# Kernel tuning notes

Hardware: AMD Instinct MI355X
Metric: run time of the kernel (lower is better)

Reference implementation:

```python
import jax, jax.numpy as jnp
import numpy as np

N = 100000
E_RAND = 400000
IN_FEATS = 512
HID = 64
HEADS = 8
NUM_CLASSES = 40
SLOPE = 0.2  # DGL GATConv leaky_relu negative_slope


def setup_inputs() -> dict:
    key = jax.random.key(0)
    ks = jax.random.split(key, 12)
    features = jax.random.normal(ks[0], (N, IN_FEATS), dtype=jnp.float32)
    src_r = jax.random.randint(ks[1], (E_RAND,), 0, N)
    dst_r = jax.random.randint(ks[2], (E_RAND,), 0, N)
    loop = jnp.arange(N)
    src = jnp.concatenate([src_r, loop]).astype(jnp.int64)
    dst = jnp.concatenate([dst_r, loop]).astype(jnp.int64)
    def glorot(k, shape, fan_in):
        return jax.random.normal(k, shape, dtype=jnp.float32) * (1.0 / np.sqrt(fan_in))
    W1 = glorot(ks[3], (IN_FEATS, HEADS * HID), IN_FEATS)
    al1 = glorot(ks[4], (HEADS, HID), HID)
    ar1 = glorot(ks[5], (HEADS, HID), HID)
    b1 = jnp.zeros((HEADS * HID,), dtype=jnp.float32)
    W2 = glorot(ks[6], (HEADS * HID, HEADS * NUM_CLASSES), HEADS * HID)
    al2 = glorot(ks[7], (HEADS, NUM_CLASSES), NUM_CLASSES)
    ar2 = glorot(ks[8], (HEADS, NUM_CLASSES), NUM_CLASSES)
    b2 = jnp.zeros((HEADS * NUM_CLASSES,), dtype=jnp.float32)
    return {"features": features, "W1": W1, "al1": al1, "ar1": ar1, "b1": b1,
            "W2": W2, "al2": al2, "ar2": ar2, "b2": b2, "src": src, "dst": dst}


def gat_conv(x, W, al, ar, b, src, dst, heads, d_out):
    # x: [N, F_in] -> feat: [N, H, D]
    n = x.shape[0]
    feat = (x @ W).reshape(n, heads, d_out)
    el = jnp.sum(feat * al, axis=-1)  # [N, H]
    er = jnp.sum(feat * ar, axis=-1)  # [N, H]
    e = jax.nn.leaky_relu(el[src] + er[dst], SLOPE)  # [E, H]
    # segment softmax over incoming edges of each destination node
    emax = jax.ops.segment_max(e, dst, num_segments=n)
    a = jnp.exp(e - emax[dst])
    asum = jax.ops.segment_sum(a, dst, num_segments=n)
    alpha = a / asum[dst]  # [E, H]
    # weighted scatter-sum of source features
    out = jax.ops.segment_sum(feat[src] * alpha[:, :, None], dst, num_segments=n)
    return out + b.reshape(1, heads, d_out)  # [N, H, D]


def reference(features, W1, al1, ar1, b1, W2, al2, ar2, b2, src, dst):
    h = gat_conv(features, W1, al1, ar1, b1, src, dst, HEADS, HID)
    h = jax.nn.relu(h.reshape(N, HEADS * HID))  # flatten(1) + relu; dropout is eval-mode identity
    out = gat_conv(h, W2, al2, ar2, b2, src, dst, HEADS, NUM_CLASSES)
    return out.mean(axis=1)  # [N, num_classes]
```

## Files before the change

kernel.cpp:

```cpp
#include <hip/hip_runtime.h>
#include <cstdint>
#include <cstddef>

#define SLOPE 0.2f
#define HEADS 8

typedef __bf16 bf16_t;
typedef __bf16 bf16x8 __attribute__((ext_vector_type(8)));
typedef float f32x4 __attribute__((ext_vector_type(4)));

__global__ void cvt_w_t(const float* __restrict__ W, bf16_t* __restrict__ Bt, int K, int N) {
  int gid = blockIdx.x * blockDim.x + threadIdx.x;
  if (gid >= K * N) return;
  int nn = gid / K, kk = gid % K;
  Bt[gid] = (bf16_t)W[(size_t)kk * N + nn];
}

__global__ void cvt_wel2(const float* __restrict__ W2, const float* __restrict__ al2,
                         const float* __restrict__ ar2, bf16_t* __restrict__ W2t) {
  int gid = blockIdx.x * blockDim.x + threadIdx.x;
  if (gid >= 8 * 512) return;
  int h = gid >> 9, k = gid & 511;
  float a = 0.f, b = 0.f;
  for (int d = 0; d < 40; ++d) {
    float w = W2[(size_t)k * 320 + h * 40 + d];
    a = fmaf(w, al2[h * 40 + d], a);
    b = fmaf(w, ar2[h * 40 + d], b);
  }
  W2t[(size_t)(320 + h) * 512 + k] = (bf16_t)a;
  W2t[(size_t)(328 + h) * 512 + k] = (bf16_t)b;
}

__global__ __launch_bounds__(256) void gemm_af32(
    const float* __restrict__ A,
    const bf16_t* __restrict__ Bt,
    bf16_t* __restrict__ Cb,
    int M, int Nc, int K) {
  __shared__ __align__(16) unsigned char lds[49152];
  const int tid = threadIdx.x;
  const int wid = tid >> 6, lane = tid & 63;
  const int wm = wid >> 1, wn = wid & 1;
  const int bm = blockIdx.y * 128, bn = blockIdx.x * 128;
  const int quad = lane >> 4, lrow = lane & 15;

  f32x4 acc[4][4] = {};

  const int arow_in = 4 * wid + (lane >> 4);
  const int acol_src = ((lane & 15) * 4) ^ (((lane >> 4) + 4 * (wid & 1)) << 3);
  const int st_sub = wid * 8 + (lane >> 3);
  const int st_k = 8 * ((lane & 7) ^ (lane >> 3));
  const bf16_t* bSrc = Bt + (size_t)(bn + st_sub) * K + st_k;

  const int xorv = (lrow & 7) << 4;
  const int aRdRow = (wm * 64 + lrow) * 256;
  const int bRdBase = (wn * 64 + lrow) * 128 + 32768;

  for (int k0 = 0; k0 < K; k0 += 64) {
    if (k0) __syncthreads();
#pragma unroll
    for (int i = 0; i < 8; ++i) {
      int rg = bm + 16 * i + arow_in;
      rg = rg < M ? rg : M - 1;
      __builtin_amdgcn_global_load_lds(
          (const __attribute__((address_space(1))) void*)(A + (size_t)rg * K + k0 + acol_src),
          (__attribute__((address_space(3))) void*)(lds + (i * 4 + wid) * 1024), 16, 0, 0);
    }
#pragma unroll
    for (int i = 0; i < 4; ++i) {
      __builtin_amdgcn_global_load_lds(
          (const __attribute__((address_space(1))) void*)(bSrc + (size_t)i * 32 * K + k0),
          (__attribute__((address_space(3))) void*)(lds + 32768 + (i * 4 + wid) * 1024), 16, 0, 0);
    }
    __syncthreads();
#pragma unroll
    for (int kk = 0; kk < 2; ++kk) {
      bf16x8 af[4], bfr[4];
      const int kbA = (kk * 128 + quad * 32) ^ ((lrow & 7) << 5);
      const int kb = (kk * 64 + quad * 16) ^ xorv;
#pragma unroll
      for (int mf = 0; mf < 4; ++mf) {
        f32x4 lo = *(const f32x4*)(lds + aRdRow + mf * 4096 + kbA);
        f32x4 hi = *(const f32x4*)(lds + aRdRow + mf * 4096 + kbA + 16);
        bf16x8 t;
        t[0] = (bf16_t)lo[0]; t[1] = (bf16_t)lo[1]; t[2] = (bf16_t)lo[2]; t[3] = (bf16_t)lo[3];
        t[4] = (bf16_t)hi[0]; t[5] = (bf16_t)hi[1]; t[6] = (bf16_t)hi[2]; t[7] = (bf16_t)hi[3];
        af[mf] = t;
      }
#pragma unroll
      for (int nf = 0; nf < 4; ++nf)
        bfr[nf] = *(const bf16x8*)(lds + bRdBase + nf * 2048 + kb);
#pragma unroll
      for (int mf = 0; mf < 4; ++mf)
#pragma unroll
        for (int nf = 0; nf < 4; ++nf)
          acc[mf][nf] =
              __builtin_amdgcn_mfma_f32_16x16x32_bf16(af[mf], bfr[nf], acc[mf][nf], 0, 0, 0);
    }
  }

  const int crow0 = bm + wm * 64 + quad * 4;
  const int ccol0 = bn + wn * 64 + lrow;
#pragma unroll
  for (int mf = 0; mf < 4; ++mf) {
#pragma unroll
    for (int r2 = 0; r2 < 4; ++r2) {
      int row = crow0 + mf * 16 + r2;
      if (row < M) {
#pragma unroll
        for (int nf = 0; nf < 4; ++nf) {
          int col = ccol0 + nf * 16;
          if (col < Nc) Cb[(size_t)row * Nc + col] = (bf16_t)acc[mf][nf][r2];
        }
      }
    }
  }
}

template <bool HASEL>
__global__ __launch_bounds__(256) void gemm_bf16(
    const bf16_t* __restrict__ A,
    const bf16_t* __restrict__ Bt,
    bf16_t* __restrict__ Cb,
    float* __restrict__ elp, float* __restrict__ erp,
    int M, int NcFeat, int K) {
  __shared__ __align__(16) unsigned char lds[32768];
  const int tid = threadIdx.x;
  const int wid = tid >> 6, lane = tid & 63;
  const int wm = wid >> 1, wn = wid & 1;
  const int bm = blockIdx.y * 128, bn = blockIdx.x * 128;
  const int quad = lane >> 4, lrow = lane & 15;

  f32x4 acc[4][4] = {};

  const int st_sub = wid * 8 + (lane >> 3);
  const int st_k = 8 * ((lane & 7) ^ (lane >> 3));
  const bf16_t* aSrc = A + (size_t)(bm + st_sub) * K + st_k;
  const bf16_t* bSrc = Bt + (size_t)(bn + st_sub) * K + st_k;

  const int xorv = (lrow & 7) << 4;
  const int aRdBase = (wm * 64 + lrow) * 128;
  const int bRdBase = (wn * 64 + lrow) * 128 + 16384;

  for (int k0 = 0; k0 < K; k0 += 64) {
    if (k0) __syncthreads();
#pragma unroll
    for (int i = 0; i < 4; ++i) {
      __builtin_amdgcn_global_load_lds(
          (const __attribute__((address_space(1))) void*)(aSrc + (size_t)i * 32 * K + k0),
          (__attribute__((address_space(3))) void*)(lds + (i * 4 + wid) * 1024), 16, 0, 0);
    }
#pragma unroll
    for (int i = 0; i < 4; ++i) {
      __builtin_amdgcn_global_load_lds(
          (const __attribute__((address_space(1))) void*)(bSrc + (size_t)i * 32 * K + k0),
          (__attribute__((address_space(3))) void*)(lds + 16384 + (i * 4 + wid) * 1024), 16, 0, 0);
    }
    __syncthreads();
#pragma unroll
    for (int kk = 0; kk < 2; ++kk) {
      bf16x8 af[4], bfr[4];
      const int kb = (kk * 64 + quad * 16) ^ xorv;
#pragma unroll
      for (int mf = 0; mf < 4; ++mf)
        af[mf] = *(const bf16x8*)(lds + aRdBase + mf * 2048 + kb);
#pragma unroll
      for (int nf = 0; nf < 4; ++nf)
        bfr[nf] = *(const bf16x8*)(lds + bRdBase + nf * 2048 + kb);
#pragma unroll
      for (int mf = 0; mf < 4; ++mf)
#pragma unroll
        for (int nf = 0; nf < 4; ++nf)
          acc[mf][nf] =
              __builtin_amdgcn_mfma_f32_16x16x32_bf16(af[mf], bfr[nf], acc[mf][nf], 0, 0, 0);
    }
  }

  const int crow0 = bm + wm * 64 + quad * 4;
  const int ccol0 = bn + wn * 64 + lrow;
#pragma unroll
  for (int mf = 0; mf < 4; ++mf) {
#pragma unroll
    for (int r2 = 0; r2 < 4; ++r2) {
      int row = crow0 + mf * 16 + r2;
      if (row < M) {
#pragma unroll
        for (int nf = 0; nf < 4; ++nf) {
          int col = ccol0 + nf * 16;
          float v = acc[mf][nf][r2];
          if (col < NcFeat) {
            Cb[(size_t)row * NcFeat + col] = (bf16_t)v;
          } else if (HASEL) {
            if (col < NcFeat + 8) elp[(size_t)row * 8 + (col - NcFeat)] = v;
            else if (col < NcFeat + 16) erp[(size_t)row * 8 + (col - NcFeat - 8)] = v;
          }
        }
      }
    }
  }
}

__global__ void el_er_b(const bf16_t* __restrict__ featb, const float* __restrict__ al,
                        const float* __restrict__ ar, float* __restrict__ el,
                        float* __restrict__ er, int n, int D) {
  int gid = blockIdx.x * blockDim.x + threadIdx.x;
  if (gid >= n * HEADS) return;
  int node = gid >> 3, h = gid & 7;
  const bf16_t* f = featb + (size_t)node * HEADS * D + h * D;
  const float* alp = al + h * D;
  const float* arp = ar + h * D;
  float a = 0.f, b = 0.f;
  for (int d = 0; d < D; d += 8) {
    bf16x8 v = *(const bf16x8*)(f + d);
#pragma unroll
    for (int i = 0; i < 8; ++i) {
      float x = (float)v[i];
      a = fmaf(x, alp[d + i], a);
      b = fmaf(x, arp[d + i], b);
    }
  }
  el[gid] = a;
  er[gid] = b;
}

__global__ void count_deg(const int* __restrict__ dst, int* __restrict__ deg, int e) {
  int gid = blockIdx.x * blockDim.x + threadIdx.x;
  if (gid < e) atomicAdd(&deg[dst[gid]], 1);
}

__global__ void scan_block(const int* __restrict__ deg, int* __restrict__ incl,
                           int* __restrict__ bsum, int n) {
  __shared__ int tmp[256];
  int t = threadIdx.x;
  int gid = blockIdx.x * 256 + t;
  int v = (gid < n) ? deg[gid] : 0;
  tmp[t] = v;
  __syncthreads();
  for (int off = 1; off < 256; off <<= 1) {
    int x = (t >= off) ? tmp[t - off] : 0;
    __syncthreads();
    tmp[t] += x;
    __syncthreads();
  }
  if (gid < n) incl[gid] = tmp[t];
  if (t == 255) bsum[blockIdx.x] = tmp[255];
}

__global__ void scan_small(const int* __restrict__ bsum, int* __restrict__ bbase, int nb) {
  __shared__ int tmp[512];
  int t = threadIdx.x;
  int v = (t < nb) ? bsum[t] : 0;
  tmp[t] = v;
  __syncthreads();
  for (int off = 1; off < 512; off <<= 1) {
    int x = (t >= off) ? tmp[t - off] : 0;
    __syncthreads();
    tmp[t] += x;
    __syncthreads();
  }
  if (t < nb) bbase[t] = tmp[t] - v;
}

__global__ void finalize_offsets(const int* __restrict__ incl, const int* __restrict__ deg,
                                 const int* __restrict__ bbase, int* __restrict__ offsets,
                                 int n) {
  int gid = blockIdx.x * blockDim.x + threadIdx.x;
  if (gid >= n) return;
  int base = bbase[gid >> 8];
  offsets[gid] = incl[gid] - deg[gid] + base;
  if (gid == n - 1) offsets[n] = incl[gid] + base;
}

__global__ void scatter_edges(const int* __restrict__ src, const int* __restrict__ dst,
                              const int* __restrict__ offsets, int* __restrict__ cursor,
                              int* __restrict__ ssrc, int e) {
  int gid = blockIdx.x * blockDim.x + threadIdx.x;
  if (gid < e) {
    int d = dst[gid];
    int p = offsets[d] + atomicAdd(&cursor[d], 1);
    ssrc[p] = src[gid];
  }
}

__device__ inline void wave_softmax_stats(const float* __restrict__ el, float er_h, int h,
                                          int strip, const int* __restrict__ ssrc, int s0,
                                          int s1, float& m, float& ss) {
  m = -INFINITY;
  ss = 0.f;
  for (int j = s0 + strip; j < s1; j += 8) {
    int s = ssrc[j];
    float x = el[s * HEADS + h] + er_h;
    x = x > 0.f ? x : SLOPE * x;
    if (x > m) {
      ss = ss * __expf(m - x) + 1.f;
      m = x;
    } else {
      ss += __expf(x - m);
    }
  }
#pragma unroll
  for (int mask = 1; mask < 8; mask <<= 1) {
    float mo = __shfl_xor(m, mask, 64);
    float so = __shfl_xor(ss, mask, 64);
    float mn = fmaxf(m, mo);
    float e1 = (m == -INFINITY) ? 0.f : __expf(m - mn);
    float e2 = (mo == -INFINITY) ? 0.f : __expf(mo - mn);
    ss = ss * e1 + so * e2;
    m = mn;
  }
}

__global__ __launch_bounds__(256) void aggregate1(
    const bf16_t* __restrict__ featb, const float* __restrict__ el,
    const float* __restrict__ er, const int* __restrict__ offsets,
    const int* __restrict__ ssrc, const float* __restrict__ bias,
    bf16_t* __restrict__ outb, int n) {
  int wid = threadIdx.x >> 6, lane = threadIdx.x & 63;
  int node = blockIdx.x * 4 + wid;
  if (node >= n) return;
  int s0 = offsets[node], s1 = offsets[node + 1];
  int h = lane >> 3, strip = lane & 7;
  float er_h = er[node * HEADS + h];
  float m, ss;
  wave_softmax_stats(el, er_h, h, strip, ssrc, s0, s1, m, ss);
  float inv_ss = 1.f / ss;

  float acc[8] = {};
  for (int j = s0; j < s1; ++j) {
    int s = ssrc[j];
    float x = el[s * HEADS + h] + er_h;
    x = x > 0.f ? x : SLOPE * x;
    float alpha = __expf(x - m) * inv_ss;
    bf16x8 fv = *(const bf16x8*)(featb + (size_t)s * 512 + lane * 8);
#pragma unroll
    for (int i = 0; i < 8; ++i) acc[i] += alpha * (float)fv[i];
  }
  bf16x8 o;
#pragma unroll
  for (int i = 0; i < 8; ++i) {
    float v = acc[i] + bias[lane * 8 + i];
    o[i] = (bf16_t)fmaxf(v, 0.f);
  }
  *(bf16x8*)(outb + (size_t)node * 512 + lane * 8) = o;
}

__global__ __launch_bounds__(256) void aggregate2(
    const bf16_t* __restrict__ featb, const float* __restrict__ el,
    const float* __restrict__ er, const int* __restrict__ offsets,
    const int* __restrict__ ssrc, const float* __restrict__ bias,
    float* __restrict__ out, int n) {
  __shared__ float red[4][320];
  int wid = threadIdx.x >> 6, lane = threadIdx.x & 63;
  int node = blockIdx.x * 4 + wid;
  if (node >= n) return;
  int s0 = offsets[node], s1 = offsets[node + 1];
  int h = lane >> 3, strip = lane & 7;
  float er_h = er[node * HEADS + h];
  float m, ss;
  wave_softmax_stats(el, er_h, h, strip, ssrc, s0, s1, m, ss);
  float inv_ss = 1.f / ss;

  int alane0 = ((lane + 0 * 64) / 40) * 8;
  int alane1 = ((lane + 1 * 64) / 40) * 8;
  int alane2 = ((lane + 2 * 64) / 40) * 8;
  int alane3 = ((lane + 3 * 64) / 40) * 8;
  int alane4 = ((lane + 4 * 64) / 40) * 8;

  float acc[5] = {};
  for (int j = s0; j < s1; ++j) {
    int s = ssrc[j];
    float x = el[s * HEADS + h] + er_h;
    x = x > 0.f ? x : SLOPE * x;
    float aown = __expf(x - m) * inv_ss;
    const bf16_t* fp = featb + (size_t)s * 320;
    acc[0] += __shfl(aown, alane0, 64) * (float)fp[lane];
    acc[1] += __shfl(aown, alane1, 64) * (float)fp[lane + 64];
    acc[2] += __shfl(aown, alane2, 64) * (float)fp[lane + 128];
    acc[3] += __shfl(aown, alane3, 64) * (float)fp[lane + 192];
    acc[4] += __shfl(aown, alane4, 64) * (float)fp[lane + 256];
  }
#pragma unroll
  for (int k = 0; k < 5; ++k) {
    int d = lane + k * 64;
    red[wid][d] = acc[k] + bias[d];
  }
  __builtin_amdgcn_wave_barrier();
  asm volatile("s_waitcnt lgkmcnt(0)" ::: "memory");
  __builtin_amdgcn_wave_barrier();
  if (lane < 40) {
    float s = 0.f;
#pragma unroll
    for (int hh = 0; hh < HEADS; ++hh) s += red[wid][hh * 40 + lane];
    out[(size_t)node * 40 + lane] = s * 0.125f;
  }
}

extern "C" void kernel_launch(void* const* d_in, const int* in_sizes, int n_in,
                              void* d_out, int out_size, void* d_ws, size_t ws_size,
                              hipStream_t stream) {
  const float* features = (const float*)d_in[0];
  const float* W1 = (const float*)d_in[1];
  const float* al1 = (const float*)d_in[2];
  const float* ar1 = (const float*)d_in[3];
  const float* b1 = (const float*)d_in[4];
  const float* W2 = (const float*)d_in[5];
  const float* al2 = (const float*)d_in[6];
  const float* ar2 = (const float*)d_in[7];
  const float* b2 = (const float*)d_in[8];
  const int* src = (const int*)d_in[9];
  const int* dst = (const int*)d_in[10];
  float* out = (float*)d_out;

  const int n = in_sizes[0] / 512;
  const int e = in_sizes[9];
  const int Mp = ((n + 127) / 128) * 128;

  char* p = (char*)d_ws;
  auto alloc = [&](size_t bytes) {
    char* r = p;
    p += (bytes + 255) & ~(size_t)255;
    return r;
  };
  bf16_t* feat1b = (bf16_t*)alloc((size_t)n * 512 * 2);
  bf16_t* feat2b = feat1b;
  bf16_t* hb = (bf16_t*)alloc((size_t)Mp * 512 * 2);
  bf16_t* W1t = (bf16_t*)alloc((size_t)512 * 512 * 2);
  bf16_t* W2t = (bf16_t*)alloc((size_t)384 * 512 * 2);
  float* el1 = (float*)alloc((size_t)n * 8 * 4);
  float* er1 = (float*)alloc((size_t)n * 8 * 4);
  float* el2 = (float*)alloc((size_t)n * 8 * 4);
  float* er2 = (float*)alloc((size_t)n * 8 * 4);
  int* deg = (int*)alloc((size_t)n * 4);
  int* cursor = (int*)alloc((size_t)n * 4);
  int* incl = (int*)alloc((size_t)n * 4);
  int* offsets = (int*)alloc((size_t)(n + 1) * 4);
  int nb = (n + 255) / 256;
  int* bsum = (int*)alloc((size_t)nb * 4);
  int* bbase = (int*)alloc((size_t)nb * 4);
  int* ssrc = (int*)alloc((size_t)e * 4);

  hipMemsetAsync(deg, 0, (size_t)n * 4, stream);
  hipMemsetAsync(cursor, 0, (size_t)n * 4, stream);
  hipMemsetAsync(hb + (size_t)n * 512, 0, (size_t)(Mp - n) * 512 * 2, stream);
  hipMemsetAsync(W2t + (size_t)336 * 512, 0, (size_t)48 * 512 * 2, stream);

  int eb = (e + 255) / 256;
  count_deg<<<eb, 256, 0, stream>>>(dst, deg, e);
  scan_block<<<nb, 256, 0, stream>>>(deg, incl, bsum, n);
  scan_small<<<1, 512, 0, stream>>>(bsum, bbase, nb);
  finalize_offsets<<<nb, 256, 0, stream>>>(incl, deg, bbase, offsets, n);
  scatter_edges<<<eb, 256, 0, stream>>>(src, dst, offsets, cursor, ssrc, e);

  cvt_w_t<<<(512 * 512 + 255) / 256, 256, 0, stream>>>(W1, W1t, 512, 512);
  cvt_w_t<<<(512 * 320 + 255) / 256, 256, 0, stream>>>(W2, W2t, 512, 320);
  cvt_wel2<<<(8 * 512 + 255) / 256, 256, 0, stream>>>(W2, al2, ar2, W2t);

  dim3 g1(512 / 128, Mp / 128);
  gemm_af32<<<g1, 256, 0, stream>>>(features, W1t, feat1b, n, 512, 512);
  el_er_b<<<(n * 8 + 255) / 256, 256, 0, stream>>>(feat1b, al1, ar1, el1, er1, n, 64);
  aggregate1<<<(n + 3) / 4, 256, 0, stream>>>(feat1b, el1, er1, offsets, ssrc, b1, hb, n);

  dim3 g2(384 / 128, Mp / 128);
  gemm_bf16<true><<<g2, 256, 0, stream>>>(hb, W2t, feat2b, el2, er2, n, 320, 512);
  aggregate2<<<(n + 3) / 4, 256, 0, stream>>>(feat2b, el2, er2, offsets, ssrc, b2, out, n);
}
```

Measured before the change: 535.9 us.

## Fuse layer-1 attention logits into GEMM epilogue and merge weight prep kernels

Computes el/er for layer 1 inside the first GEMM's epilogue by dotting the fp32 accumulators with al/ar and reducing across 16 lanes with shuffles. This removes the separate el_er_b kernel and its re-read of feat1b. The three weight-conversion kernels are merged into one launch to cut launch overhead. The A-tile LDS swizzle is also changed, with matching read offsets, to alter bank-conflict behavior. Logits now come from fp32 accumulators instead of bf16-rounded features, which slightly changes numerics.

Measured after the change: 513.8 us. 1.04x faster.

```diff
diff --git a/kernel.cpp b/kernel.cpp
--- a/kernel.cpp
+++ b/kernel.cpp
@@ -9,32 +9,37 @@
 typedef __bf16 bf16x8 __attribute__((ext_vector_type(8)));
 typedef float f32x4 __attribute__((ext_vector_type(4)));
 
-__global__ void cvt_w_t(const float* __restrict__ W, bf16_t* __restrict__ Bt, int K, int N) {
+__global__ void prep_weights(const float* __restrict__ W1, const float* __restrict__ W2,
+                             const float* __restrict__ al2, const float* __restrict__ ar2,
+                             bf16_t* __restrict__ W1t, bf16_t* __restrict__ W2t) {
   int gid = blockIdx.x * blockDim.x + threadIdx.x;
-  if (gid >= K * N) return;
-  int nn = gid / K, kk = gid % K;
-  Bt[gid] = (bf16_t)W[(size_t)kk * N + nn];
-}
-
-__global__ void cvt_wel2(const float* __restrict__ W2, const float* __restrict__ al2,
-                         const float* __restrict__ ar2, bf16_t* __restrict__ W2t) {
-  int gid = blockIdx.x * blockDim.x + threadIdx.x;
-  if (gid >= 8 * 512) return;
-  int h = gid >> 9, k = gid & 511;
-  float a = 0.f, b = 0.f;
-  for (int d = 0; d < 40; ++d) {
-    float w = W2[(size_t)k * 320 + h * 40 + d];
-    a = fmaf(w, al2[h * 40 + d], a);
-    b = fmaf(w, ar2[h * 40 + d], b);
-  }
-  W2t[(size_t)(320 + h) * 512 + k] = (bf16_t)a;
-  W2t[(size_t)(328 + h) * 512 + k] = (bf16_t)b;
+  if (gid < 512 * 512) {
+    int nn = gid >> 9, kk = gid & 511;
+    W1t[gid] = (bf16_t)W1[(size_t)kk * 512 + nn];
+  } else if (gid < 512 * 512 + 320 * 512) {
+    int g = gid - 512 * 512;
+    int nn = g >> 9, kk = g & 511;
+    W2t[g] = (bf16_t)W2[(size_t)kk * 320 + nn];
+  } else if (gid < 512 * 512 + 320 * 512 + 8 * 512) {
+    int g = gid - (512 * 512 + 320 * 512);
+    int h = g >> 9, k = g & 511;
+    float a = 0.f, b = 0.f;
+    for (int d = 0; d < 40; ++d) {
+      float w = W2[(size_t)k * 320 + h * 40 + d];
+      a = fmaf(w, al2[h * 40 + d], a);
+      b = fmaf(w, ar2[h * 40 + d], b);
+    }
+    W2t[(size_t)(320 + h) * 512 + k] = (bf16_t)a;
+    W2t[(size_t)(328 + h) * 512 + k] = (bf16_t)b;
+  }
 }
 
 __global__ __launch_bounds__(256) void gemm_af32(
     const float* __restrict__ A,
     const bf16_t* __restrict__ Bt,
     bf16_t* __restrict__ Cb,
+    const float* __restrict__ al, const float* __restrict__ ar,
+    float* __restrict__ elp, float* __restrict__ erp,
     int M, int Nc, int K) {
   __shared__ __align__(16) unsigned char lds[49152];
   const int tid = threadIdx.x;
@@ -46,12 +51,12 @@
   f32x4 acc[4][4] = {};
 
   const int arow_in = 4 * wid + (lane >> 4);
-  const int acol_src = ((lane & 15) * 4) ^ (((lane >> 4) + 4 * (wid & 1)) << 3);
+  const int acol_src = ((lane & 15) * 4) ^ ((4 * (wid & 1) + (lane >> 4)) << 2);
   const int st_sub = wid * 8 + (lane >> 3);
   const int st_k = 8 * ((lane & 7) ^ (lane >> 3));
   const bf16_t* bSrc = Bt + (size_t)(bn + st_sub) * K + st_k;
 
-  const int xorv = (lrow & 7) << 4;
+  const int x16 = (lrow & 7) << 4;
   const int aRdRow = (wm * 64 + lrow) * 256;
   const int bRdBase = (wn * 64 + lrow) * 128 + 32768;
 
@@ -75,12 +80,12 @@
 #pragma unroll
     for (int kk = 0; kk < 2; ++kk) {
       bf16x8 af[4], bfr[4];
-      const int kbA = (kk * 128 + quad * 32) ^ ((lrow & 7) << 5);
-      const int kb = (kk * 64 + quad * 16) ^ xorv;
+      const int slotB = kk * 128 + quad * 32;
+      const int kb = (kk * 64 + quad * 16) ^ x16;
 #pragma unroll
       for (int mf = 0; mf < 4; ++mf) {
-        f32x4 lo = *(const f32x4*)(lds + aRdRow + mf * 4096 + kbA);
-        f32x4 hi = *(const f32x4*)(lds + aRdRow + mf * 4096 + kbA + 16);
+        f32x4 lo = *(const f32x4*)(lds + aRdRow + mf * 4096 + (slotB ^ x16));
+        f32x4 hi = *(const f32x4*)(lds + aRdRow + mf * 4096 + ((slotB + 16) ^ x16));
         bf16x8 t;
         t[0] = (bf16_t)lo[0]; t[1] = (bf16_t)lo[1]; t[2] = (bf16_t)lo[2]; t[3] = (bf16_t)lo[3];
         t[4] = (bf16_t)hi[0]; t[5] = (bf16_t)hi[1]; t[6] = (bf16_t)hi[2]; t[7] = (bf16_t)hi[3];
@@ -114,10 +119,42 @@
       }
     }
   }
-}
-
-template <bool HASEL>
-__global__ __launch_bounds__(256) void gemm_bf16(
+
+  {
+    const int hh = (bn >> 6) + wn;
+    float alv[4], arv[4];
+#pragma unroll
+    for (int nf = 0; nf < 4; ++nf) {
+      alv[nf] = al[hh * 64 + lrow + nf * 16];
+      arv[nf] = ar[hh * 64 + lrow + nf * 16];
+    }
+#pragma unroll
+    for (int mf = 0; mf < 4; ++mf) {
+#pragma unroll
+      for (int r2 = 0; r2 < 4; ++r2) {
+        float pe = 0.f, pr = 0.f;
+#pragma unroll
+        for (int nf = 0; nf < 4; ++nf) {
+          float v = acc[mf][nf][r2];
+          pe = fmaf(v, alv[nf], pe);
+          pr = fmaf(v, arv[nf], pr);
+        }
+#pragma unroll
+        for (int mask = 1; mask < 16; mask <<= 1) {
+          pe += __shfl_xor(pe, mask, 64);
+          pr += __shfl_xor(pr, mask, 64);
+        }
+        int row = crow0 + mf * 16 + r2;
+        if (lrow == 0 && row < M) {
+          elp[(size_t)row * 8 + hh] = pe;
+          erp[(size_t)row * 8 + hh] = pr;
+        }
+      }
+    }
+  }
+}
+
+__global__ __launch_bounds__(256) void gemm_bf16_l2(
     const bf16_t* __restrict__ A,
     const bf16_t* __restrict__ Bt,
     bf16_t* __restrict__ Cb,
@@ -189,37 +226,15 @@
           float v = acc[mf][nf][r2];
           if (col < NcFeat) {
             Cb[(size_t)row * NcFeat + col] = (bf16_t)v;
-          } else if (HASEL) {
-            if (col < NcFeat + 8) elp[(size_t)row * 8 + (col - NcFeat)] = v;
-            else if (col < NcFeat + 16) erp[(size_t)row * 8 + (col - NcFeat - 8)] = v;
+          } else if (col < NcFeat + 8) {
+            elp[(size_t)row * 8 + (col - NcFeat)] = v;
+          } else if (col < NcFeat + 16) {
+            erp[(size_t)row * 8 + (col - NcFeat - 8)] = v;
           }
         }
       }
     }
   }
-}
-
-__global__ void el_er_b(const bf16_t* __restrict__ featb, const float* __restrict__ al,
-                        const float* __restrict__ ar, float* __restrict__ el,
-                        float* __restrict__ er, int n, int D) {
-  int gid = blockIdx.x * blockDim.x + threadIdx.x;
-  if (gid >= n * HEADS) return;
-  int node = gid >> 3, h = gid & 7;
-  const bf16_t* f = featb + (size_t)node * HEADS * D + h * D;
-  const float* alp = al + h * D;
-  const float* arp = ar + h * D;
-  float a = 0.f, b = 0.f;
-  for (int d = 0; d < D; d += 8) {
-    bf16x8 v = *(const bf16x8*)(f + d);
-#pragma unroll
-    for (int i = 0; i < 8; ++i) {
-      float x = (float)v[i];
-      a = fmaf(x, alp[d + i], a);
-      b = fmaf(x, arp[d + i], b);
-    }
-  }
-  el[gid] = a;
-  er[gid] = b;
 }
 
 __global__ void count_deg(const int* __restrict__ dst, int* __restrict__ deg, int e) {
@@ -450,16 +465,14 @@
   finalize_offsets<<<nb, 256, 0, stream>>>(incl, deg, bbase, offsets, n);
   scatter_edges<<<eb, 256, 0, stream>>>(src, dst, offsets, cursor, ssrc, e);
 
-  cvt_w_t<<<(512 * 512 + 255) / 256, 256, 0, stream>>>(W1, W1t, 512, 512);
-  cvt_w_t<<<(512 * 320 + 255) / 256, 256, 0, stream>>>(W2, W2t, 512, 320);
-  cvt_wel2<<<(8 * 512 + 255) / 256, 256, 0, stream>>>(W2, al2, ar2, W2t);
+  prep_weights<<<(512 * 512 + 320 * 512 + 8 * 512 + 255) / 256, 256, 0, stream>>>(
+      W1, W2, al2, ar2, W1t, W2t);
 
   dim3 g1(512 / 128, Mp / 128);
-  gemm_af32<<<g1, 256, 0, stream>>>(features, W1t, feat1b, n, 512, 512);
-  el_er_b<<<(n * 8 + 255) / 256, 256, 0, stream>>>(feat1b, al1, ar1, el1, er1, n, 64);
+  gemm_af32<<<g1, 256, 0, stream>>>(features, W1t, feat1b, al1, ar1, el1, er1, n, 512, 512);
   aggregate1<<<(n + 3) / 4, 256, 0, stream>>>(feat1b, el1, er1, offsets, ssrc, b1, hb, n);
 
   dim3 g2(384 / 128, Mp / 128);
-  gemm_bf16<true><<<g2, 256, 0, stream>>>(hb, W2t, feat2b, el2, er2, n, 320, 512);
+  gemm_bf16_l2<<<g2, 256, 0, stream>>>(hb, W2t, feat2b, el2, er2, n, 320, 512);
   aggregate2<<<(n + 3) / 4, 256, 0, stream>>>(feat2b, el2, er2, offsets, ssrc, b2, out, n);
 }
```
